# Kernel optimization log

Measured on AMD Instinct MI355X. Metric: run time of the kernel, lower is better.

Reference implementation:

```python
import jax, jax.numpy as jnp
import numpy as np

D = 1024
H = 16
HD = D // H
EPS = 1e-5


def setup_inputs() -> dict:
    key = jax.random.key(0)
    ks = jax.random.split(key, 8)
    s_in = 1.0 / np.sqrt(D)
    s_ff = 1.0 / np.sqrt(4 * D)
    return {
        "x": jax.random.normal(ks[0], (2, 2048, D), dtype=jnp.float32),
        "w_qkv": jax.random.uniform(ks[1], (D, 3 * D), minval=-s_in, maxval=s_in, dtype=jnp.float32),
        "b_qkv": jnp.zeros((3 * D,), jnp.float32),
        "w_out": jax.random.uniform(ks[2], (D, D), minval=-s_in, maxval=s_in, dtype=jnp.float32),
        "b_out": jnp.zeros((D,), jnp.float32),
        "w_ff1": jax.random.uniform(ks[3], (D, 4 * D), minval=-s_in, maxval=s_in, dtype=jnp.float32),
        "b_ff1": jnp.zeros((4 * D,), jnp.float32),
        "w_ff2": jax.random.uniform(ks[4], (4 * D, D), minval=-s_ff, maxval=s_ff, dtype=jnp.float32),
        "b_ff2": jnp.zeros((D,), jnp.float32),
        "gamma1": jnp.ones((D,), jnp.float32),
        "beta1": jnp.zeros((D,), jnp.float32),
        "gamma2": jnp.ones((D,), jnp.float32),
        "beta2": jnp.zeros((D,), jnp.float32),
    }


def _layer_norm(x, gamma, beta):
    mean = jnp.mean(x, axis=-1, keepdims=True)
    var = jnp.var(x, axis=-1, keepdims=True, ddof=1)  # torch.var is unbiased
    return (x - mean) / jnp.sqrt(var + EPS) * gamma + beta


def reference(x, w_qkv, b_qkv, w_out, b_out, w_ff1, b_ff1, w_ff2, b_ff2,
              gamma1, beta1, gamma2, beta2):
    B, C, _ = x.shape
    qkv = x @ w_qkv + b_qkv                     # [B,C,3D]
    q, k, v = jnp.split(qkv, 3, axis=-1)
    # [B,C,D] -> [B,H,C,hd]
    q = q.reshape(B, C, H, HD).transpose(0, 2, 1, 3)
    k = k.reshape(B, C, H, HD).transpose(0, 2, 1, 3)
    v = v.reshape(B, C, H, HD).transpose(0, 2, 1, 3)
    attn = jnp.einsum('bhid,bhjd->bhij', q, k) / np.sqrt(HD).astype(np.float32)
    attn = jax.nn.softmax(attn, axis=-1)
    h_attn = jnp.einsum('bhij,bhjd->bhid', attn, v)
    h_attn = h_attn.transpose(0, 2, 1, 3).reshape(B, C, D)
    h_attn = h_attn @ w_out + b_out
    h_attn = _layer_norm(h_attn + x, gamma1, beta1)
    h_ff = jax.nn.gelu(h_attn @ w_ff1 + b_ff1, approximate=False) @ w_ff2 + b_ff2
    return _layer_norm(h_ff + h_attn, gamma2, beta2)
```

## Files before the change

### kernel.cpp

```cpp
#include <hip/hip_runtime.h>
#include <hip/hip_bf16.h>
#include <math.h>

#define DDIM 1024
#define HHD  64
#define NH   16
#define BB   2
#define CTX  2048
#define MROWS (BB*CTX)
#define D3   (3*DDIM)
#define DF   (4*DDIM)

using bf16x8 = __attribute__((ext_vector_type(8))) short;
using f32x4  = __attribute__((ext_vector_type(4))) float;
using f32x16 = __attribute__((ext_vector_type(16))) float;

__device__ __forceinline__ unsigned short f2bf(float f) {
  union { float f; unsigned u; } c; c.f = f;
  unsigned u = c.u;
  return (unsigned short)((u + 0x7FFFu + ((u >> 16) & 1u)) >> 16);
}

__device__ __forceinline__ unsigned pk2(float a, float b) {
  __hip_bfloat162 h = __float22bfloat162_rn(float2{a, b});
  return *reinterpret_cast<unsigned*>(&h);
}

__device__ __forceinline__ float asf(unsigned u) {
  union { unsigned u; float f; } c; c.u = u; return c.f;
}

__device__ __forceinline__ float4 bf4(uint2 u) {
  float4 r;
  r.x = asf(u.x << 16);
  r.y = asf(u.x & 0xffff0000u);
  r.z = asf(u.y << 16);
  r.w = asf(u.y & 0xffff0000u);
  return r;
}

__device__ __forceinline__ void pl32swap(unsigned &a, unsigned &b) {
  asm volatile("v_permlane32_swap_b32 %0, %1" : "+v"(a), "+v"(b));
}

__device__ __forceinline__ void gload16(const void* g, void* l) {
  __builtin_amdgcn_global_load_lds(
      (const __attribute__((address_space(1))) unsigned int*)g,
      (__attribute__((address_space(3))) unsigned int*)l, 16, 0, 0);
}

template<int N>
__device__ __forceinline__ void vmwait() {
  if constexpr (N == 0)      asm volatile("s_waitcnt vmcnt(0)" ::: "memory");
  else if constexpr (N == 3) asm volatile("s_waitcnt vmcnt(3)" ::: "memory");
  else if constexpr (N == 4) asm volatile("s_waitcnt vmcnt(4)" ::: "memory");
  else if constexpr (N == 6) asm volatile("s_waitcnt vmcnt(6)" ::: "memory");
  else static_assert(N != N, "add vmcnt literal");
}

__device__ __forceinline__ float fast_gelu(float x) {
  float u = x * fmaf(0.10294817f, x * x, 2.3022072f);
  u = fminf(fmaxf(u, -80.f), 80.f);
  float t = __builtin_amdgcn_exp2f(u);
  return x * t * __builtin_amdgcn_rcpf(t + 1.0f);
}

__global__ void k_prep(const float* __restrict__ x, unsigned short* __restrict__ Xb,
                       const float* __restrict__ w_qkv, unsigned short* __restrict__ WqkvT,
                       const float* __restrict__ w_out, unsigned short* __restrict__ WoutT,
                       const float* __restrict__ w_ff1, unsigned short* __restrict__ Wff1T,
                       const float* __restrict__ w_ff2, unsigned short* __restrict__ Wff2T) {
  __shared__ float tile[32][33];
  const int bid = blockIdx.x, t = threadIdx.x;
  if (bid < 4096) {
    int i = bid * 256 + t;
    float4 v = reinterpret_cast<const float4*>(x)[i];
    uint2 o;
    o.x = pk2(v.x, v.y); o.y = pk2(v.z, v.w);
    reinterpret_cast<uint2*>(Xb)[i] = o;
    return;
  }
  const float* in; unsigned short* out; int R, Cn, bx, by;
  if (bid < 7168)       { int k = bid - 4096;  in = w_qkv; out = WqkvT; R = DDIM; Cn = D3;   bx = k % (D3/32); by = k / (D3/32); }
  else if (bid < 8192)  { int k = bid - 7168;  in = w_out; out = WoutT; R = DDIM; Cn = DDIM; bx = k % 32;      by = k / 32; }
  else if (bid < 12288) { int k = bid - 8192;  in = w_ff1; out = Wff1T; R = DDIM; Cn = DF;   bx = k % (DF/32); by = k / (DF/32); }
  else                  { int k = bid - 12288; in = w_ff2; out = Wff2T; R = DF;   Cn = DDIM; bx = k % 32;      by = k / 32; }
  const int c0 = bx * 32, r0 = by * 32;
  const int tr = t >> 5, tc = t & 31;
#pragma unroll
  for (int i = 0; i < 4; ++i)
    tile[tr + i*8][tc] = in[(size_t)(r0 + tr + i*8) * Cn + (c0 + tc)];
  __syncthreads();
#pragma unroll
  for (int i = 0; i < 4; ++i)
    out[(size_t)(c0 + tr + i*8) * R + (r0 + tc)] = f2bf(tile[tc][tr + i*8]);
}

__global__ void k_transpose_v(const unsigned short* __restrict__ in, unsigned short* __restrict__ out) {
  __shared__ unsigned short tile[32][33];
  int head = blockIdx.z;
  int d0 = blockIdx.x * 32, c0 = blockIdx.y * 32;
  int t = threadIdx.x, tr = t >> 5, tc = t & 31;
  const unsigned short* ip = in + (size_t)head * CTX * HHD;
  unsigned short* op = out + (size_t)head * CTX * HHD;
#pragma unroll
  for (int i = 0; i < 4; ++i)
    tile[tr + i*8][tc] = ip[(c0 + tr + i*8) * HHD + (d0 + tc)];
  __syncthreads();
#pragma unroll
  for (int i = 0; i < 4; ++i)
    op[(d0 + tr + i*8) * CTX + (c0 + tc)] = tile[tc][tr + i*8];
}

template<int EPI, int BM, int BN, int WSM, int WSN, int OCC, int SPLITK = 1>
__launch_bounds__(WSM*WSN*64, OCC)
__global__ void k_gemm(const unsigned short* __restrict__ A,
                       const unsigned short* __restrict__ Bt,
                       const float* __restrict__ bias,
                       const float* __restrict__ res,
                       float* __restrict__ outf,
                       unsigned short* __restrict__ outb,
                       unsigned short* __restrict__ outQ,
                       unsigned short* __restrict__ outK,
                       unsigned short* __restrict__ outV,
                       int Ndim, int Kdim) {
  constexpr int THREADS = WSM * WSN * 64;
  constexpr int WM = BM / (WSM * 16);
  constexpr int WN = BN / (WSN * 16);
  constexpr int LA = (BM * 4) / THREADS;
  constexpr int LB = (BN * 4) / THREADS;
  constexpr int L  = LA + LB;
  constexpr int NBUF = 3;

  __shared__ __align__(16) unsigned short As[NBUF][BM * 32];
  __shared__ __align__(16) unsigned short Bs[NBUF][BN * 32];

  const int nwg = gridDim.x * gridDim.y;
  const int lin = blockIdx.y * gridDim.x + blockIdx.x;
  const int swz = (lin & 7) * (nwg >> 3) + (lin >> 3);
  const int m0 = (swz / gridDim.x) * BM, n0 = (swz % gridDim.x) * BN;

  const int Kc = Kdim / SPLITK;
  const size_t koff = (size_t)blockIdx.z * Kc;

  const int t = threadIdx.x;
  const int w = t >> 6, lane = t & 63, lr = lane & 15, lg = lane >> 4;
  const int wr = (w / WSN) * (WM * 16);
  const int wc = (w % WSN) * (WN * 16);

  f32x4 acc[WM][WN];
#pragma unroll
  for (int i = 0; i < WM; ++i)
#pragma unroll
    for (int j = 0; j < WN; ++j) acc[i][j] = f32x4{0.f, 0.f, 0.f, 0.f};

  const int srow = t >> 2;
  const int sgr  = (t & 3) ^ ((t >> 3) & 3);
  const unsigned short* Asrc[LA];
  const unsigned short* Bsrc[LB];
#pragma unroll
  for (int i = 0; i < LA; ++i)
    Asrc[i] = A + (size_t)(m0 + i * (THREADS / 4) + srow) * Kdim + koff + sgr * 8;
#pragma unroll
  for (int i = 0; i < LB; ++i)
    Bsrc[i] = Bt + (size_t)(n0 + i * (THREADS / 4) + srow) * Kdim + koff + sgr * 8;

  int offA[WM], offB[WN];
#pragma unroll
  for (int mi = 0; mi < WM; ++mi) {
    int r = wr + mi * 16 + lr;
    offA[mi] = r * 32 + ((lg ^ ((r >> 1) & 3)) * 8);
  }
#pragma unroll
  for (int ni = 0; ni < WN; ++ni) {
    int r = wc + ni * 16 + lr;
    offB[ni] = r * 32 + ((lg ^ ((r >> 1) & 3)) * 8);
  }

#define STAGE(buf, ko)                                                   \
  do {                                                                   \
    _Pragma("unroll")                                                    \
    for (int i = 0; i < LA; ++i)                                         \
      gload16(Asrc[i] + (ko), &As[buf][(i * THREADS + t) * 8]);          \
    _Pragma("unroll")                                                    \
    for (int i = 0; i < LB; ++i)                                         \
      gload16(Bsrc[i] + (ko), &Bs[buf][(i * THREADS + t) * 8]);          \
  } while (0)

  STAGE(0, 0);
  STAGE(1, 32);

  const int nk = Kc >> 5;
  int rd = 0, tgt = 2;
  for (int kk = 0; kk < nk; ++kk) {
    if (kk + 1 < nk) vmwait<L>(); else vmwait<0>();
    __builtin_amdgcn_s_barrier();
    asm volatile("" ::: "memory");
    if (kk + 2 < nk) STAGE(tgt, (kk + 2) * 32);

    bf16x8 af[WM], bfr[WN];
#pragma unroll
    for (int mi = 0; mi < WM; ++mi) af[mi]  = *(const bf16x8*)&As[rd][offA[mi]];
#pragma unroll
    for (int ni = 0; ni < WN; ++ni) bfr[ni] = *(const bf16x8*)&Bs[rd][offB[ni]];
#pragma unroll
    for (int mi = 0; mi < WM; ++mi)
#pragma unroll
      for (int ni = 0; ni < WN; ++ni)
        acc[mi][ni] = __builtin_amdgcn_mfma_f32_16x16x32_bf16(af[mi], bfr[ni], acc[mi][ni], 0, 0, 0);
    rd  = (rd == 2)  ? 0 : rd + 1;
    tgt = (tgt == 2) ? 0 : tgt + 1;
  }
#undef STAGE

  unsigned short* cpw = nullptr;
  if constexpr (EPI == 3)
    cpw = (blockIdx.z == 0) ? (unsigned short*)outf : outb;

#pragma unroll
  for (int mi = 0; mi < WM; ++mi) {
#pragma unroll
    for (int r = 0; r < 4; ++r) {
      int row = m0 + wr + mi * 16 + lg * 4 + r;
#pragma unroll
      for (int ni = 0; ni < WN; ++ni) {
        int col = n0 + wc + ni * 16 + lr;
        float v = acc[mi][ni][r];
        if constexpr (EPI != 3) v += bias[col];
        if constexpr (EPI == 0) {
          int b = row >> 11, c = row & 2047;
          int sec = col >> 10, nn = col & 1023;
          int h = nn >> 6, d = nn & 63;
          size_t o = ((size_t)(b * NH + h) * CTX + c) * HHD + d;
          if (sec == 0) outQ[o] = f2bf(v * 0.18033688f);
          else if (sec == 1) outK[o] = f2bf(v);
          else outV[o] = f2bf(v);
        } else if constexpr (EPI == 1) {
          size_t o = (size_t)row * Ndim + col;
          outf[o] = v + res[o];
        } else if constexpr (EPI == 2) {
          outb[(size_t)row * Ndim + col] = f2bf(fast_gelu(v));
        } else {
          cpw[(size_t)row * Ndim + col] = f2bf(v);
        }
      }
    }
  }
}

__launch_bounds__(256, 2)
__global__ void k_attn(const unsigned short* __restrict__ Qb,
                       const unsigned short* __restrict__ Kb,
                       const unsigned short* __restrict__ Vt,
                       unsigned short* __restrict__ A2) {
  __shared__ __align__(16) unsigned short Ks[2][64 * 64];
  __shared__ __align__(16) unsigned short Vs[2][64 * 64];
  const int lin = blockIdx.x;
  const int blk = (lin & 7) * 64 + (lin >> 3);
  const int bh = blk >> 4;
  const int qt = blk & 15;
  const int b = bh >> 4, h = bh & 15;
  const int t = threadIdx.x, w = t >> 6, lane = t & 63;
  const int li = lane & 31, hi = lane >> 5;
  const int qbase = qt * 128 + w * 32;
  const unsigned short* Qh = Qb + (size_t)bh * CTX * HHD;
  const unsigned short* Kh = Kb + (size_t)bh * CTX * HHD;
  const unsigned short* Vh = Vt + (size_t)bh * CTX * HHD;

  const int srow = t >> 3, sgr = (t & 7) ^ ((t >> 3) & 7);
  const unsigned short* Kg0 = Kh + srow * HHD + sgr * 8;
  const unsigned short* Kg1 = Kg0 + 32 * HHD;
  const unsigned short* Vg0 = Vh + (size_t)srow * CTX + sgr * 8;
  const unsigned short* Vg1 = Vg0 + (size_t)32 * CTX;

#define STAGEKV(buf, j0)                              \
  do {                                                \
    gload16(Kg0 + (j0) * HHD, &Ks[buf][t * 8]);       \
    gload16(Kg1 + (j0) * HHD, &Ks[buf][(256 + t) * 8]); \
    gload16(Vg0 + (j0), &Vs[buf][t * 8]);             \
    gload16(Vg1 + (j0), &Vs[buf][(256 + t) * 8]);     \
  } while (0)

  int fo[2][4];
#pragma unroll
  for (int x = 0; x < 2; ++x)
#pragma unroll
    for (int y = 0; y < 4; ++y)
      fo[x][y] = (x*32 + li) * 64 + (((2*y + hi) ^ (li & 7)) * 8);

  bf16x8 aq[4];
#pragma unroll
  for (int kt = 0; kt < 4; ++kt)
    aq[kt] = *(const bf16x8*)(Qh + (qbase + li) * HHD + kt * 16 + hi * 8);

  bf16x8 ones;
#pragma unroll
  for (int i = 0; i < 8; ++i) ones[i] = (short)0x3F80;

  STAGEKV(0, 0);

  f32x16 oacc0, oacc1, lacc;
#pragma unroll
  for (int r = 0; r < 16; ++r) { oacc0[r] = 0.f; oacc1[r] = 0.f; lacc[r] = 0.f; }

  __syncthreads();

  int cur = 0;
  for (int j0 = 0; j0 < CTX; j0 += 64) {
    if (j0 + 64 < CTX) STAGEKV(cur ^ 1, j0 + 64);

    f32x16 s0, s1;
#pragma unroll
    for (int r = 0; r < 16; ++r) { s0[r] = 0.f; s1[r] = 0.f; }
    __builtin_amdgcn_s_setprio(1);
#pragma unroll
    for (int kt = 0; kt < 4; ++kt) {
      bf16x8 kf0 = *(const bf16x8*)&Ks[cur][fo[0][kt]];
      bf16x8 kf1 = *(const bf16x8*)&Ks[cur][fo[1][kt]];
      s0 = __builtin_amdgcn_mfma_f32_32x32x16_bf16(kf0, aq[kt], s0, 0, 0, 0);
      s1 = __builtin_amdgcn_mfma_f32_32x32x16_bf16(kf1, aq[kt], s1, 0, 0, 0);
    }
    __builtin_amdgcn_s_setprio(0);

#pragma unroll
    for (int r = 0; r < 16; ++r) {
      s0[r] = __builtin_amdgcn_exp2f(s0[r]);
      s1[r] = __builtin_amdgcn_exp2f(s1[r]);
    }

    unsigned u0[2][4], u1[2][4];
#pragma unroll
    for (int g = 0; g < 4; ++g) {
      u0[0][g] = pk2(s0[4*g], s0[4*g+1]);
      u1[0][g] = pk2(s0[4*g+2], s0[4*g+3]);
      u0[1][g] = pk2(s1[4*g], s1[4*g+1]);
      u1[1][g] = pk2(s1[4*g+2], s1[4*g+3]);
    }

    __builtin_amdgcn_s_setprio(1);
#pragma unroll
    for (int jt16 = 0; jt16 < 4; ++jt16) {
      const int jt2 = jt16 >> 1, a2 = (jt16 & 1) * 2;
      unsigned x0 = u0[jt2][a2 + 1], y0 = u0[jt2][a2];
      unsigned x1 = u1[jt2][a2 + 1], y1 = u1[jt2][a2];
      pl32swap(x0, y0);
      pl32swap(x1, y1);
      union { unsigned u[4]; bf16x8 v; } pf;
      pf.u[0] = y0; pf.u[1] = y1; pf.u[2] = x0; pf.u[3] = x1;
      bf16x8 vf0 = *(const bf16x8*)&Vs[cur][fo[0][jt16]];
      bf16x8 vf1 = *(const bf16x8*)&Vs[cur][fo[1][jt16]];
      oacc0 = __builtin_amdgcn_mfma_f32_32x32x16_bf16(vf0, pf.v, oacc0, 0, 0, 0);
      oacc1 = __builtin_amdgcn_mfma_f32_32x32x16_bf16(vf1, pf.v, oacc1, 0, 0, 0);
      lacc  = __builtin_amdgcn_mfma_f32_32x32x16_bf16(ones, pf.v, lacc, 0, 0, 0);
    }
    __builtin_amdgcn_s_setprio(0);
    __syncthreads();
    cur ^= 1;
  }
#undef STAGEKV

  float rinv = 1.0f / lacc[0];

  size_t rowbase = ((size_t)(b * CTX + qbase + li)) * DDIM + h * HHD;
#pragma unroll
  for (int q = 0; q < 4; ++q) {
    uint2 ov;
    ov.x = pk2(oacc0[4*q] * rinv, oacc0[4*q+1] * rinv);
    ov.y = pk2(oacc0[4*q+2] * rinv, oacc0[4*q+3] * rinv);
    *(uint2*)&A2[rowbase + q*8 + hi*4] = ov;
    ov.x = pk2(oacc1[4*q] * rinv, oacc1[4*q+1] * rinv);
    ov.y = pk2(oacc1[4*q+2] * rinv, oacc1[4*q+3] * rinv);
    *(uint2*)&A2[rowbase + 32 + q*8 + hi*4] = ov;
  }
}

template<bool WB>
__global__ void k_lnred(const unsigned short* __restrict__ c0, const unsigned short* __restrict__ c1,
                        const float* __restrict__ bias, const float* __restrict__ res,
                        const float* __restrict__ gamma, const float* __restrict__ beta,
                        float* __restrict__ outf, unsigned short* __restrict__ outb) {
  const int row = blockIdx.x, t = threadIdx.x;
  const size_t o4 = (size_t)row * (DDIM / 4) + t;
  float4 f0 = bf4(reinterpret_cast<const uint2*>(c0)[o4]);
  float4 f1 = bf4(reinterpret_cast<const uint2*>(c1)[o4]);
  float4 rr = reinterpret_cast<const float4*>(res)[o4];
  float4 bi = reinterpret_cast<const float4*>(bias)[t];
  float4 v;
  v.x = (f0.x + f1.x) + bi.x + rr.x;
  v.y = (f0.y + f1.y) + bi.y + rr.y;
  v.z = (f0.z + f1.z) + bi.z + rr.z;
  v.w = (f0.w + f1.w) + bi.w + rr.w;
  float s  = (v.x + v.y) + (v.z + v.w);
  float sq = (v.x*v.x + v.y*v.y) + (v.z*v.z + v.w*v.w);
#pragma unroll
  for (int off = 1; off < 64; off <<= 1) { s += __shfl_xor(s, off); sq += __shfl_xor(sq, off); }
  __shared__ float red[2][4];
  int w = t >> 6;
  if ((t & 63) == 0) { red[0][w] = s; red[1][w] = sq; }
  __syncthreads();
  s  = red[0][0] + red[0][1] + red[0][2] + red[0][3];
  sq = red[1][0] + red[1][1] + red[1][2] + red[1][3];
  float mean = s * (1.0f / DDIM);
  float var  = (sq - s * mean) * (1.0f / (DDIM - 1));
  float rstd = rsqrtf(var + 1e-5f);
  float4 gm = reinterpret_cast<const float4*>(gamma)[t];
  float4 bt = reinterpret_cast<const float4*>(beta)[t];
  float4 o;
  o.x = (v.x - mean) * rstd * gm.x + bt.x;
  o.y = (v.y - mean) * rstd * gm.y + bt.y;
  o.z = (v.z - mean) * rstd * gm.z + bt.z;
  o.w = (v.w - mean) * rstd * gm.w + bt.w;
  reinterpret_cast<float4*>(outf + (size_t)row * DDIM)[t] = o;
  if constexpr (WB) {
    uint2 p; p.x = pk2(o.x, o.y); p.y = pk2(o.z, o.w);
    reinterpret_cast<uint2*>(outb + (size_t)row * DDIM)[t] = p;
  }
}

extern "C" void kernel_launch(void* const* d_in, const int* in_sizes, int n_in,
                              void* d_out, int out_size, void* d_ws, size_t ws_size,
                              hipStream_t stream) {
  const float* x      = (const float*)d_in[0];
  const float* w_qkv  = (const float*)d_in[1];
  const float* b_qkv  = (const float*)d_in[2];
  const float* w_out  = (const float*)d_in[3];
  const float* b_out  = (const float*)d_in[4];
  const float* w_ff1  = (const float*)d_in[5];
  const float* b_ff1  = (const float*)d_in[6];
  const float* w_ff2  = (const float*)d_in[7];
  const float* b_ff2  = (const float*)d_in[8];
  const float* gamma1 = (const float*)d_in[9];
  const float* beta1  = (const float*)d_in[10];
  const float* gamma2 = (const float*)d_in[11];
  const float* beta2  = (const float*)d_in[12];
  float* out = (float*)d_out;

  char* ws = (char*)d_ws;
  const size_t MB = 1024ull * 1024ull;
  unsigned short* Xb    = (unsigned short*)(ws + 0);
  unsigned short* WqkvT = (unsigned short*)(ws + 8*MB);
  unsigned short* WoutT = (unsigned short*)(ws + 14*MB);
  unsigned short* Wff1T = (unsigned short*)(ws + 16*MB);
  unsigned short* Wff2T = (unsigned short*)(ws + 24*MB);
  unsigned short* Qb    = (unsigned short*)(ws + 32*MB);
  unsigned short* Kb    = (unsigned short*)(ws + 40*MB);
  unsigned short* Vt    = (unsigned short*)(ws + 48*MB);
  unsigned short* A2    = (unsigned short*)(ws + 56*MB);
  unsigned short* Vb    = (unsigned short*)(ws + 56*MB);
  unsigned short* G     = (unsigned short*)(ws + 32*MB);
  float* h1f            = (float*)(ws + 64*MB);
  unsigned short* h1b   = (unsigned short*)(ws + 80*MB);
  unsigned short* Cp1_0 = (unsigned short*)(ws + 88*MB);
  unsigned short* Cp1_1 = (unsigned short*)(ws + 96*MB);
  unsigned short* Cp2_0 = (unsigned short*)(ws + 0);
  unsigned short* Cp2_1 = (unsigned short*)(ws + 8*MB);

  k_prep<<<dim3(16384), dim3(256), 0, stream>>>(
      x, Xb, w_qkv, WqkvT, w_out, WoutT, w_ff1, Wff1T, w_ff2, Wff2T);

  k_gemm<0, 256, 128, 4, 2, 2><<<dim3(D3/128, MROWS/256), dim3(512), 0, stream>>>(
      Xb, WqkvT, b_qkv, nullptr, nullptr, nullptr, Qb, Kb, Vb, D3, DDIM);
  k_transpose_v<<<dim3(HHD/32, CTX/32, BB*NH), dim3(256), 0, stream>>>(Vb, Vt);

  k_attn<<<dim3(BB*NH*(CTX/128)), dim3(256), 0, stream>>>(Qb, Kb, Vt, A2);

  k_gemm<3, 128, 128, 2, 2, 3, 2><<<dim3(DDIM/128, MROWS/128, 2), dim3(256), 0, stream>>>(
      A2, WoutT, nullptr, nullptr, (float*)Cp1_0, Cp1_1, nullptr, nullptr, nullptr,
      DDIM, DDIM);
  k_lnred<true><<<dim3(MROWS), dim3(256), 0, stream>>>(
      Cp1_0, Cp1_1, b_out, x, gamma1, beta1, h1f, h1b);

  k_gemm<2, 256, 128, 4, 2, 2><<<dim3(DF/128, MROWS/256), dim3(512), 0, stream>>>(
      h1b, Wff1T, b_ff1, nullptr, nullptr, G, nullptr, nullptr, nullptr, DF, DDIM);

  k_gemm<3, 128, 128, 2, 2, 3, 2><<<dim3(DDIM/128, MROWS/128, 2), dim3(256), 0, stream>>>(
      G, Wff2T, nullptr, nullptr, (float*)Cp2_0, Cp2_1, nullptr, nullptr, nullptr,
      DDIM, DF);
  k_lnred<false><<<dim3(MROWS), dim3(256), 0, stream>>>(
      Cp2_0, Cp2_1, b_ff2, h1f, gamma2, beta2, out, nullptr);
}
```

Before: 236.8 us.

## Double per-wave query tile in attention kernel to reuse K/V tiles

Each wave now processes two 32-row query subtiles against every staged K/V tile, so a block covers 256 queries and the grid is halved. This halves the global K/V loads and LDS staging per query and amortises the barriers and shared-memory fragment reads over twice the MFMA work. In exchange, register pressure roughly doubles (launch bounds drop to one block per SIMD target), and the smaller grid leaves fewer waves per CU to hide latency.

```diff
diff --git a/kernel.cpp b/kernel.cpp
--- a/kernel.cpp
+++ b/kernel.cpp
@@ -248,7 +248,7 @@
   }
 }
 
-__launch_bounds__(256, 2)
+__launch_bounds__(256, 1)
 __global__ void k_attn(const unsigned short* __restrict__ Qb,
                        const unsigned short* __restrict__ Kb,
                        const unsigned short* __restrict__ Vt,
@@ -256,13 +256,13 @@
   __shared__ __align__(16) unsigned short Ks[2][64 * 64];
   __shared__ __align__(16) unsigned short Vs[2][64 * 64];
   const int lin = blockIdx.x;
-  const int blk = (lin & 7) * 64 + (lin >> 3);
-  const int bh = blk >> 4;
-  const int qt = blk & 15;
+  const int blk = (lin & 7) * 32 + (lin >> 3);
+  const int bh = blk >> 3;
+  const int qt = blk & 7;
   const int b = bh >> 4, h = bh & 15;
   const int t = threadIdx.x, w = t >> 6, lane = t & 63;
   const int li = lane & 31, hi = lane >> 5;
-  const int qbase = qt * 128 + w * 32;
+  const int qbase = qt * 256 + w * 64;
   const unsigned short* Qh = Qb + (size_t)bh * CTX * HHD;
   const unsigned short* Kh = Kb + (size_t)bh * CTX * HHD;
   const unsigned short* Vh = Vt + (size_t)bh * CTX * HHD;
@@ -288,10 +288,12 @@
     for (int y = 0; y < 4; ++y)
       fo[x][y] = (x*32 + li) * 64 + (((2*y + hi) ^ (li & 7)) * 8);
 
-  bf16x8 aq[4];
-#pragma unroll
-  for (int kt = 0; kt < 4; ++kt)
-    aq[kt] = *(const bf16x8*)(Qh + (qbase + li) * HHD + kt * 16 + hi * 8);
+  bf16x8 aq0[4], aq1[4];
+#pragma unroll
+  for (int kt = 0; kt < 4; ++kt) {
+    aq0[kt] = *(const bf16x8*)(Qh + (qbase + li) * HHD + kt * 16 + hi * 8);
+    aq1[kt] = *(const bf16x8*)(Qh + (qbase + 32 + li) * HHD + kt * 16 + hi * 8);
+  }
 
   bf16x8 ones;
 #pragma unroll
@@ -299,9 +301,12 @@
 
   STAGEKV(0, 0);
 
-  f32x16 oacc0, oacc1, lacc;
-#pragma unroll
-  for (int r = 0; r < 16; ++r) { oacc0[r] = 0.f; oacc1[r] = 0.f; lacc[r] = 0.f; }
+  f32x16 oa00, oa01, oa10, oa11, la0, la1;
+#pragma unroll
+  for (int r = 0; r < 16; ++r) {
+    oa00[r] = 0.f; oa01[r] = 0.f; oa10[r] = 0.f; oa11[r] = 0.f;
+    la0[r] = 0.f; la1[r] = 0.f;
+  }
 
   __syncthreads();
 
@@ -309,49 +314,67 @@
   for (int j0 = 0; j0 < CTX; j0 += 64) {
     if (j0 + 64 < CTX) STAGEKV(cur ^ 1, j0 + 64);
 
-    f32x16 s0, s1;
-#pragma unroll
-    for (int r = 0; r < 16; ++r) { s0[r] = 0.f; s1[r] = 0.f; }
+    f32x16 s00, s01, s10, s11;
+#pragma unroll
+    for (int r = 0; r < 16; ++r) { s00[r] = 0.f; s01[r] = 0.f; s10[r] = 0.f; s11[r] = 0.f; }
     __builtin_amdgcn_s_setprio(1);
 #pragma unroll
     for (int kt = 0; kt < 4; ++kt) {
       bf16x8 kf0 = *(const bf16x8*)&Ks[cur][fo[0][kt]];
       bf16x8 kf1 = *(const bf16x8*)&Ks[cur][fo[1][kt]];
-      s0 = __builtin_amdgcn_mfma_f32_32x32x16_bf16(kf0, aq[kt], s0, 0, 0, 0);
-      s1 = __builtin_amdgcn_mfma_f32_32x32x16_bf16(kf1, aq[kt], s1, 0, 0, 0);
+      s00 = __builtin_amdgcn_mfma_f32_32x32x16_bf16(kf0, aq0[kt], s00, 0, 0, 0);
+      s01 = __builtin_amdgcn_mfma_f32_32x32x16_bf16(kf1, aq0[kt], s01, 0, 0, 0);
+      s10 = __builtin_amdgcn_mfma_f32_32x32x16_bf16(kf0, aq1[kt], s10, 0, 0, 0);
+      s11 = __builtin_amdgcn_mfma_f32_32x32x16_bf16(kf1, aq1[kt], s11, 0, 0, 0);
     }
     __builtin_amdgcn_s_setprio(0);
 
 #pragma unroll
     for (int r = 0; r < 16; ++r) {
-      s0[r] = __builtin_amdgcn_exp2f(s0[r]);
-      s1[r] = __builtin_amdgcn_exp2f(s1[r]);
+      s00[r] = __builtin_amdgcn_exp2f(s00[r]);
+      s01[r] = __builtin_amdgcn_exp2f(s01[r]);
+      s10[r] = __builtin_amdgcn_exp2f(s10[r]);
+      s11[r] = __builtin_amdgcn_exp2f(s11[r]);
     }
 
-    unsigned u0[2][4], u1[2][4];
+    unsigned uA0[2][4], uB0[2][4], uA1[2][4], uB1[2][4];
 #pragma unroll
     for (int g = 0; g < 4; ++g) {
-      u0[0][g] = pk2(s0[4*g], s0[4*g+1]);
-      u1[0][g] = pk2(s0[4*g+2], s0[4*g+3]);
-      u0[1][g] = pk2(s1[4*g], s1[4*g+1]);
-      u1[1][g] = pk2(s1[4*g+2], s1[4*g+3]);
+      uA0[0][g] = pk2(s00[4*g], s00[4*g+1]);
+      uB0[0][g] = pk2(s00[4*g+2], s00[4*g+3]);
+      uA0[1][g] = pk2(s01[4*g], s01[4*g+1]);
+      uB0[1][g] = pk2(s01[4*g+2], s01[4*g+3]);
+      uA1[0][g] = pk2(s10[4*g], s10[4*g+1]);
+      uB1[0][g] = pk2(s10[4*g+2], s10[4*g+3]);
+      uA1[1][g] = pk2(s11[4*g], s11[4*g+1]);
+      uB1[1][g] = pk2(s11[4*g+2], s11[4*g+3]);
     }
 
     __builtin_amdgcn_s_setprio(1);
 #pragma unroll
     for (int jt16 = 0; jt16 < 4; ++jt16) {
       const int jt2 = jt16 >> 1, a2 = (jt16 & 1) * 2;
-      unsigned x0 = u0[jt2][a2 + 1], y0 = u0[jt2][a2];
-      unsigned x1 = u1[jt2][a2 + 1], y1 = u1[jt2][a2];
+      unsigned x0 = uA0[jt2][a2 + 1], y0 = uA0[jt2][a2];
+      unsigned x1 = uB0[jt2][a2 + 1], y1 = uB0[jt2][a2];
       pl32swap(x0, y0);
       pl32swap(x1, y1);
-      union { unsigned u[4]; bf16x8 v; } pf;
-      pf.u[0] = y0; pf.u[1] = y1; pf.u[2] = x0; pf.u[3] = x1;
+      union { unsigned u[4]; bf16x8 v; } pf0;
+      pf0.u[0] = y0; pf0.u[1] = y1; pf0.u[2] = x0; pf0.u[3] = x1;
+      unsigned x2 = uA1[jt2][a2 + 1], y2 = uA1[jt2][a2];
+      unsigned x3 = uB1[jt2][a2 + 1], y3 = uB1[jt2][a2];
+      pl32swap(x2, y2);
+      pl32swap(x3, y3);
+      union { unsigned u[4]; bf16x8 v; } pf1;
+      pf1.u[0] = y2; pf1.u[1] = y3; pf1.u[2] = x2; pf1.u[3] = x3;
+
       bf16x8 vf0 = *(const bf16x8*)&Vs[cur][fo[0][jt16]];
       bf16x8 vf1 = *(const bf16x8*)&Vs[cur][fo[1][jt16]];
-      oacc0 = __builtin_amdgcn_mfma_f32_32x32x16_bf16(vf0, pf.v, oacc0, 0, 0, 0);
-      oacc1 = __builtin_amdgcn_mfma_f32_32x32x16_bf16(vf1, pf.v, oacc1, 0, 0, 0);
-      lacc  = __builtin_amdgcn_mfma_f32_32x32x16_bf16(ones, pf.v, lacc, 0, 0, 0);
+      oa00 = __builtin_amdgcn_mfma_f32_32x32x16_bf16(vf0, pf0.v, oa00, 0, 0, 0);
+      oa01 = __builtin_amdgcn_mfma_f32_32x32x16_bf16(vf1, pf0.v, oa01, 0, 0, 0);
+      oa10 = __builtin_amdgcn_mfma_f32_32x32x16_bf16(vf0, pf1.v, oa10, 0, 0, 0);
+      oa11 = __builtin_amdgcn_mfma_f32_32x32x16_bf16(vf1, pf1.v, oa11, 0, 0, 0);
+      la0  = __builtin_amdgcn_mfma_f32_32x32x16_bf16(ones, pf0.v, la0, 0, 0, 0);
+      la1  = __builtin_amdgcn_mfma_f32_32x32x16_bf16(ones, pf1.v, la1, 0, 0, 0);
     }
     __builtin_amdgcn_s_setprio(0);
     __syncthreads();
@@ -359,18 +382,26 @@
   }
 #undef STAGEKV
 
-  float rinv = 1.0f / lacc[0];
-
-  size_t rowbase = ((size_t)(b * CTX + qbase + li)) * DDIM + h * HHD;
+  float rinv0 = 1.0f / la0[0];
+  float rinv1 = 1.0f / la1[0];
+
+  size_t rb0 = ((size_t)(b * CTX + qbase + li)) * DDIM + h * HHD;
+  size_t rb1 = ((size_t)(b * CTX + qbase + 32 + li)) * DDIM + h * HHD;
 #pragma unroll
   for (int q = 0; q < 4; ++q) {
     uint2 ov;
-    ov.x = pk2(oacc0[4*q] * rinv, oacc0[4*q+1] * rinv);
-    ov.y = pk2(oacc0[4*q+2] * rinv, oacc0[4*q+3] * rinv);
-    *(uint2*)&A2[rowbase + q*8 + hi*4] = ov;
-    ov.x = pk2(oacc1[4*q] * rinv, oacc1[4*q+1] * rinv);
-    ov.y = pk2(oacc1[4*q+2] * rinv, oacc1[4*q+3] * rinv);
-    *(uint2*)&A2[rowbase + 32 + q*8 + hi*4] = ov;
+    ov.x = pk2(oa00[4*q] * rinv0, oa00[4*q+1] * rinv0);
+    ov.y = pk2(oa00[4*q+2] * rinv0, oa00[4*q+3] * rinv0);
+    *(uint2*)&A2[rb0 + q*8 + hi*4] = ov;
+    ov.x = pk2(oa01[4*q] * rinv0, oa01[4*q+1] * rinv0);
+    ov.y = pk2(oa01[4*q+2] * rinv0, oa01[4*q+3] * rinv0);
+    *(uint2*)&A2[rb0 + 32 + q*8 + hi*4] = ov;
+    ov.x = pk2(oa10[4*q] * rinv1, oa10[4*q+1] * rinv1);
+    ov.y = pk2(oa10[4*q+2] * rinv1, oa10[4*q+3] * rinv1);
+    *(uint2*)&A2[rb1 + q*8 + hi*4] = ov;
+    ov.x = pk2(oa11[4*q] * rinv1, oa11[4*q+1] * rinv1);
+    ov.y = pk2(oa11[4*q+2] * rinv1, oa11[4*q+3] * rinv1);
+    *(uint2*)&A2[rb1 + 32 + q*8 + hi*4] = ov;
   }
 }
 
@@ -462,7 +493,7 @@
       Xb, WqkvT, b_qkv, nullptr, nullptr, nullptr, Qb, Kb, Vb, D3, DDIM);
   k_transpose_v<<<dim3(HHD/32, CTX/32, BB*NH), dim3(256), 0, stream>>>(Vb, Vt);
 
-  k_attn<<<dim3(BB*NH*(CTX/128)), dim3(256), 0, stream>>>(Qb, Kb, Vt, A2);
+  k_attn<<<dim3(BB*NH*(CTX/256)), dim3(256), 0, stream>>>(Qb, Kb, Vt, A2);
 
   k_gemm<3, 128, 128, 2, 2, 3, 2><<<dim3(DDIM/128, MROWS/128, 2), dim3(256), 0, stream>>>(
       A2, WoutT, nullptr, nullptr, (float*)Cp1_0, Cp1_1, nullptr, nullptr, nullptr,
```

Result: slower. 255.9 us (+8.1%).
